# Kernel optimization log

Measured on AMD Instinct MI355X. Metric: run time of the kernel, lower is better.

Reference implementation:

```python
import jax, jax.numpy as jnp
import numpy as np
from jax import lax

B, N, T = 64, 50, 30          # batch, history length, words per title
VOCAB, E = 50000, 300          # vocab size, word emb dim
FN, A, G, K = 400, 200, 400, 3 # filter_num, attention_dim, gru_unit, window size
USERS = 50000


def setup_inputs() -> dict:
    key = jax.random.key(0)
    ks = jax.random.split(key, 12)
    return {
        "user_id": jax.random.randint(ks[0], (B,), 0, USERS),
        "history_title": jax.random.randint(ks[1], (B, N, T), 0, VOCAB),
        "history_length": jax.random.randint(ks[2], (B,), 1, N + 1),
        "word_emb": jax.random.normal(ks[3], (VOCAB, E), jnp.float32) * 0.02,
        "conv_w": jax.random.normal(ks[4], (K, E, FN), jnp.float32) * 0.05,  # WIO layout
        "conv_b": jnp.zeros((FN,), jnp.float32),
        "v": jax.random.normal(ks[5], (FN, A), jnp.float32) * 0.05,
        "vb": jnp.zeros((A,), jnp.float32),
        "q": jax.random.normal(ks[6], (A, 1), jnp.float32) * 0.05,
        "user_emb": jax.random.normal(ks[7], (USERS, G), jnp.float32) * 0.02,
        "W_ih": jax.random.normal(ks[8], (3 * G, FN), jnp.float32) * 0.05,
        "W_hh": jax.random.normal(ks[9], (3 * G, G), jnp.float32) * 0.05,
        "b_ih": jnp.zeros((3 * G,), jnp.float32),
        "b_hh": jnp.zeros((3 * G,), jnp.float32),
    }


def _news_encode(history_title, word_emb, conv_w, conv_b, v, vb, q):
    # word embedding lookup: [B, N, T, E] (dropout is identity in eval mode)
    W = word_emb[history_title]
    # Conv1d over the word axis, padding=1 keeps length T
    x = W.reshape(B * N, T, E)
    C = lax.conv_general_dilated(
        x, conv_w, window_strides=(1,), padding=[(1, 1)],
        dimension_numbers=("NWC", "WIO", "NWC")) + conv_b
    C = jax.nn.relu(C).reshape(B, N, T, FN)
    # additive attention scores
    a = jnp.tanh(jnp.einsum("bntf,fa->bnta", C, v) + vb)
    a = jnp.einsum("bnta,ao->bnt", a, q)  # q: [A,1] -> squeeze
    # original uses Softmax(dim=0) on a [n, t] per sample => over the n-titles axis
    alpha = jax.nn.softmax(a, axis=1)
    # e[i] = alpha[i] @ C[i]: weighted sum over words -> [B, N, FN]
    return jnp.einsum("bnt,bntf->bnf", alpha, C)


def _gru(news_embed, h0, lengths, W_ih, W_hh, b_ih, b_hh):
    # packed_padded semantics: h stops updating once step >= length
    xs = jnp.swapaxes(news_embed, 0, 1)                 # [N, B, FN]
    mask = jnp.arange(N)[:, None] < lengths[None, :]    # [N, B]

    def step(h, inp):
        x_t, m = inp
        gx = x_t @ W_ih.T + b_ih                        # [B, 3G]
        gh = h @ W_hh.T + b_hh
        xr, xz, xn = jnp.split(gx, 3, axis=-1)
        hr, hz, hn = jnp.split(gh, 3, axis=-1)
        r = jax.nn.sigmoid(xr + hr)
        z = jax.nn.sigmoid(xz + hz)
        n = jnp.tanh(xn + r * hn)
        h_new = (1.0 - z) * n + z * h
        h = jnp.where(m[:, None], h_new, h)
        return h, None

    h_final, _ = lax.scan(step, h0, (xs, mask))
    return h_final


def reference(user_id, history_title, history_length, word_emb, conv_w, conv_b,
              v, vb, q, user_emb, W_ih, W_hh, b_ih, b_hh):
    news_embed = _news_encode(history_title, word_emb, conv_w, conv_b, v, vb, q)
    h0 = user_emb[user_id]                              # [B, G]
    return _gru(news_embed, h0, history_length, W_ih, W_hh, b_ih, b_hh)
```

## Files before the change

### kernel.cpp

```cpp
#include <hip/hip_runtime.h>
#include <hip/hip_bf16.h>

#define BB 64
#define NN 50
#define TT 30
#define EE 300
#define FN 400
#define AA 200
#define GG 400

typedef __attribute__((ext_vector_type(8))) short bf16x8;
typedef __attribute__((ext_vector_type(4))) float f32x4;

__device__ inline ushort f2bf(float x) {
  __hip_bfloat16 b = __float2bfloat16(x);
  return *(ushort*)&b;
}

__global__ void k_prep_all(
    const float* __restrict__ Whh, const float* __restrict__ cw,
    const float* __restrict__ v, const float* __restrict__ q,
    const float* __restrict__ vb, const float* __restrict__ Wih,
    const int* __restrict__ user_id, const float* __restrict__ user_emb,
    float* __restrict__ Wpack, __hip_bfloat16* __restrict__ WT2,
    __hip_bfloat16* __restrict__ vT2, float* __restrict__ qp,
    float* __restrict__ vbp, __hip_bfloat16* __restrict__ Wih_bf,
    float* __restrict__ h0)
{
  int i = blockIdx.x * 256 + threadIdx.x;
  if (i < 480000) {
    int jl = i % 150;
    int g = (i / 150) % 400;
    int gc = i / 60000;
    int gate = jl / 50, gl = jl - gate * 50;
    int j = gate * 400 + gc * 50 + gl;
    Wpack[i] = Whh[j * 400 + g];
  } else if (i < 910080) {
    int k = i - 480000;
    int kk = k & 31, f = (k >> 5) % 448, s = k / (448 * 32);
    int ko = s / 10, e = (s - ko * 10) * 32 + kk;
    float val = (f < FN && e < EE) ? cw[(ko * EE + e) * FN + f] : 0.f;
    WT2[k] = __float2bfloat16(val);
  } else if (i < 1003264) {
    int k = i - 910080;
    int kk = k & 31, a = (k >> 5) % 224, ks = k / (224 * 32);
    int e = ks * 32 + kk;
    float val = (a < AA && e < FN) ? v[e * AA + a] : 0.f;
    vT2[k] = __float2bfloat16(val);
  } else if (i < 1003488) {
    int k = i - 1003264;
    qp[k]  = k < AA ? q[k]  : 0.f;
    vbp[k] = k < AA ? vb[k] : 0.f;
  } else if (i < 1562592) {
    int k = i - 1003488;
    int j = k / 416, f = k % 416;
    Wih_bf[k] = __float2bfloat16((j < 1200 && f < FN) ? Wih[j * 400 + f] : 0.f);
  } else if (i < 1588192) {
    int k = i - 1562592;
    int b = k / GG, g = k - b * GG;
    h0[k] = user_emb[(size_t)user_id[b] * GG + g];
  }
}

__global__ void k_prep_emb(const float* __restrict__ w, __hip_bfloat16* __restrict__ o) {
  int i = blockIdx.x * 256 + threadIdx.x;
  if (i < 50000 * 80) {
    int row = i / 80, cg = i - row * 80;
    ushort4 u4 = make_ushort4(0, 0, 0, 0);
    if (cg < 75) {
      float4 v4 = *(const float4*)(w + (size_t)row * EE + cg * 4);
      u4 = make_ushort4(f2bf(v4.x), f2bf(v4.y), f2bf(v4.z), f2bf(v4.w));
    }
    *(ushort4*)((ushort*)o + (size_t)row * 320 + cg * 4) = u4;
  }
}

__global__ __launch_bounds__(256, 2) void k_conv(
    const int* __restrict__ title, const __hip_bfloat16* __restrict__ emb,
    const __hip_bfloat16* __restrict__ WT2, const float* __restrict__ conv_b,
    __hip_bfloat16* __restrict__ C)
{
  __shared__ __align__(16) ushort E[2][34][332];
  __shared__ int words[60];
  const int g = blockIdx.x;
  const int tid = threadIdx.x;
  const int lane = tid & 63, wn = tid >> 6;
  const int l15 = lane & 15, l4 = lane >> 4;

  if (tid < 60) words[tid] = title[g * 60 + tid];
  for (int idx = tid; idx < 2822; idx += 256)
    *(uint4*)((ushort*)E + idx * 8) = make_uint4(0u, 0u, 0u, 0u);
  __syncthreads();
  for (int idx = tid; idx < 2400; idx += 256) {
    int row = idx / 40, c = idx - row * 40;
    int tt = row / 30, w = row - tt * 30;
    *(uint4*)(&E[tt][w + 1][c * 8]) =
        *(const uint4*)((const ushort*)emb + (size_t)words[row] * 320 + c * 8);
  }
  __syncthreads();

  f32x4 acc[4][7];
#pragma unroll
  for (int nt = 0; nt < 7; ++nt) {
    int f = wn * 112 + nt * 16 + l15;
    float bj = (f < FN) ? conv_b[f] : 0.f;
#pragma unroll
    for (int mt = 0; mt < 4; ++mt) {
      acc[mt][nt][0] = bj; acc[mt][nt][1] = bj;
      acc[mt][nt][2] = bj; acc[mt][nt][3] = bj;
    }
  }

  const ushort* Bbase = (const ushort*)WT2 + (size_t)(wn * 112 + l15) * 32 + l4 * 8;

#pragma unroll
  for (int ko = 0; ko < 3; ++ko) {
#pragma unroll
    for (int ks = 0; ks < 10; ++ks) {
      const int s = ko * 10 + ks;
      bf16x8 bq[7];
#pragma unroll
      for (int nt = 0; nt < 7; ++nt)
        bq[nt] = *(const bf16x8*)(Bbase + (size_t)s * 14336 + nt * 512);
      bf16x8 af[4];
#pragma unroll
      for (int mt = 0; mt < 4; ++mt)
        af[mt] = *(const bf16x8*)(&E[mt >> 1][(mt & 1) * 16 + l15 + ko][ks * 32 + l4 * 8]);
#pragma unroll
      for (int nt = 0; nt < 7; ++nt)
#pragma unroll
        for (int mt = 0; mt < 4; ++mt)
          acc[mt][nt] = __builtin_amdgcn_mfma_f32_16x16x32_bf16(af[mt], bq[nt], acc[mt][nt], 0, 0, 0);
    }
  }

#pragma unroll
  for (int mt = 0; mt < 4; ++mt) {
    const int ti = mt >> 1;
    const int tb = (mt & 1) * 16 + l4 * 4;
#pragma unroll
    for (int nt = 0; nt < 7; ++nt) {
      int f = wn * 112 + nt * 16 + l15;
      if (f < 416) {
#pragma unroll
        for (int r = 0; r < 4; ++r) {
          int t = tb + r;
          if (t < TT) {
            float vv = fmaxf(acc[mt][nt][r], 0.f);
            C[((size_t)(g * 2 + ti) * 30 + t) * 416 + f] = __float2bfloat16(vv);
          }
        }
      }
    }
  }
}

__global__ __launch_bounds__(512) void k_attn(
    const __hip_bfloat16* __restrict__ C, const __hip_bfloat16* __restrict__ vT2,
    const float* __restrict__ vbp, const float* __restrict__ qp,
    float* __restrict__ score)
{
  __shared__ float sred[2][256];
  const int tid = threadIdx.x;
  const int lane = tid & 63, wid = tid >> 6;
  const int wm = wid >> 1, wn = wid & 1;
  const int l15 = lane & 15, l4 = lane >> 4;
  const size_t row0 = (size_t)blockIdx.x * 256;

  f32x4 acc[4][7];
  float ql[7];
#pragma unroll
  for (int nt = 0; nt < 7; ++nt) {
    int a = wn * 112 + nt * 16 + l15;
    ql[nt] = qp[a];
    float vbv = vbp[a];
#pragma unroll
    for (int mt = 0; mt < 4; ++mt) {
      acc[mt][nt][0] = vbv; acc[mt][nt][1] = vbv;
      acc[mt][nt][2] = vbv; acc[mt][nt][3] = vbv;
    }
  }

  const ushort* Vbase = (const ushort*)vT2 + (size_t)(wn * 112 + l15) * 32 + l4 * 8;
  const ushort* Cbase = (const ushort*)C + (row0 + wm * 64 + l15) * 416 + l4 * 8;

  for (int ks = 0; ks < 13; ++ks) {
    bf16x8 vf[7];
#pragma unroll
    for (int nt = 0; nt < 7; ++nt)
      vf[nt] = *(const bf16x8*)(Vbase + ((size_t)ks * 224 + nt * 16) * 32);
    bf16x8 cf[4];
#pragma unroll
    for (int mt = 0; mt < 4; ++mt)
      cf[mt] = *(const bf16x8*)(Cbase + (size_t)mt * 16 * 416 + ks * 32);
#pragma unroll
    for (int nt = 0; nt < 7; ++nt)
#pragma unroll
      for (int mt = 0; mt < 4; ++mt)
        acc[mt][nt] = __builtin_amdgcn_mfma_f32_16x16x32_bf16(cf[mt], vf[nt], acc[mt][nt], 0, 0, 0);
  }

  float sums[4][4];
#pragma unroll
  for (int mt = 0; mt < 4; ++mt)
#pragma unroll
    for (int r = 0; r < 4; ++r) sums[mt][r] = 0.f;
#pragma unroll
  for (int mt = 0; mt < 4; ++mt)
#pragma unroll
    for (int nt = 0; nt < 7; ++nt)
#pragma unroll
      for (int r = 0; r < 4; ++r)
        sums[mt][r] += tanhf(acc[mt][nt][r]) * ql[nt];
#pragma unroll
  for (int mask = 1; mask < 16; mask <<= 1)
#pragma unroll
    for (int mt = 0; mt < 4; ++mt)
#pragma unroll
      for (int r = 0; r < 4; ++r)
        sums[mt][r] += __shfl_xor(sums[mt][r], mask);

  float outv = 0.f;
#pragma unroll
  for (int mt = 0; mt < 4; ++mt)
#pragma unroll
    for (int r = 0; r < 4; ++r)
      if (l15 == mt * 4 + r) outv = sums[mt][r];
  sred[wn][wm * 64 + (l15 >> 2) * 16 + l4 * 4 + (l15 & 3)] = outv;
  __syncthreads();
  if (tid < 256) score[row0 + tid] = sred[0][tid] + sred[1][tid];
}

__global__ void k2_softmax_n(const float* __restrict__ score, float* __restrict__ alpha) {
  int i = blockIdx.x * 256 + threadIdx.x;
  if (i >= BB * TT) return;
  int b = i / TT, t = i - b * TT;
  int base = b * (NN * TT) + t;
  float m = -1e30f;
  for (int n = 0; n < NN; ++n) m = fmaxf(m, score[base + n * TT]);
  float s = 0.f;
  for (int n = 0; n < NN; ++n) s += __expf(score[base + n * TT] - m);
  float inv = 1.f / s;
  for (int n = 0; n < NN; ++n)
    alpha[base + n * TT] = __expf(score[base + n * TT] - m) * inv;
}

__global__ __launch_bounds__(256) void k3_wsum(
    const float* __restrict__ alpha, const __hip_bfloat16* __restrict__ C,
    __hip_bfloat16* __restrict__ Ebf) {
  __shared__ float al[TT];
  const int bn = blockIdx.x;
  const int tid = threadIdx.x;
  if (tid < TT) al[tid] = alpha[bn * TT + tid];
  __syncthreads();
  for (int f = tid; f < 416; f += 256) {
    float s = 0.f;
    if (f < FN) {
#pragma unroll
      for (int t = 0; t < TT; ++t)
        s = fmaf(al[t], __bfloat162float(C[((size_t)bn * TT + t) * 416 + f]), s);
    }
    Ebf[(size_t)bn * 416 + f] = __float2bfloat16(s);
  }
}

__global__ __launch_bounds__(512) void k4_gx_mfma(
    const __hip_bfloat16* __restrict__ Ebf,
    const __hip_bfloat16* __restrict__ Wih,
    const float* __restrict__ b_ih,
    float* __restrict__ gx)
{
  __shared__ __align__(16) ushort Alds[128 * 40];
  __shared__ __align__(16) ushort Blds[448 * 40];
  const int tid = threadIdx.x;
  const int lane = tid & 63, wid = tid >> 6;
  const int wm = wid >> 2, wn = wid & 3;
  const int l15 = lane & 15, l4 = lane >> 4;
  const int mb = blockIdx.x / 3;
  const int nb = blockIdx.x - mb * 3;
  const int row0 = mb * 128;
  const int n0 = nb * 448;

  f32x4 acc[4][7];
#pragma unroll
  for (int nt = 0; nt < 7; ++nt) {
    int j = n0 + wn * 112 + nt * 16 + l15;
    float bj = (j < 1200) ? b_ih[j] : 0.f;
#pragma unroll
    for (int mt = 0; mt < 4; ++mt) {
      acc[mt][nt][0] = bj; acc[mt][nt][1] = bj;
      acc[mt][nt][2] = bj; acc[mt][nt][3] = bj;
    }
  }

  const int ar = tid >> 2, ac = tid & 3;
  for (int ks = 0; ks < 13; ++ks) {
    *(uint4*)(&Alds[ar * 40 + ac * 8]) =
        *(const uint4*)((const ushort*)Ebf + (size_t)(row0 + ar) * 416 + ks * 32 + ac * 8);
    for (int idx = tid; idx < 1792; idx += 512) {
      int r = idx >> 2, c = idx & 3;
      *(uint4*)(&Blds[r * 40 + c * 8]) =
          *(const uint4*)((const ushort*)Wih + (size_t)(n0 + r) * 416 + ks * 32 + c * 8);
    }
    __syncthreads();
    bf16x8 af[4];
#pragma unroll
    for (int mt = 0; mt < 4; ++mt)
      af[mt] = *(const bf16x8*)(&Alds[(wm * 64 + mt * 16 + l15) * 40 + l4 * 8]);
#pragma unroll
    for (int nt = 0; nt < 7; ++nt) {
      bf16x8 bfr = *(const bf16x8*)(&Blds[(wn * 112 + nt * 16 + l15) * 40 + l4 * 8]);
#pragma unroll
      for (int mt = 0; mt < 4; ++mt)
        acc[mt][nt] = __builtin_amdgcn_mfma_f32_16x16x32_bf16(af[mt], bfr, acc[mt][nt], 0, 0, 0);
    }
    __syncthreads();
  }

#pragma unroll
  for (int mt = 0; mt < 4; ++mt) {
    int row = row0 + wm * 64 + mt * 16 + l4 * 4;
#pragma unroll
    for (int nt = 0; nt < 7; ++nt) {
      int j = n0 + wn * 112 + nt * 16 + l15;
      if (j < 1200) {
#pragma unroll
        for (int r = 0; r < 4; ++r)
          gx[(size_t)(row + r) * 1200 + j] = acc[mt][nt][r];
      }
    }
  }
}

__global__ __launch_bounds__(256) void k5_step(
    const float* __restrict__ h_prev, float* __restrict__ h_next,
    const float* __restrict__ Wpack, const float* __restrict__ b_hh,
    const float* __restrict__ gx, const int* __restrict__ hist_len,
    float* __restrict__ out, int step)
{
  const int gc = blockIdx.x & 7;
  const int bg = blockIdx.x >> 3;
  const int tid = threadIdx.x;
  __shared__ float ghl[2][3][50];

  if (tid < 150) {
    const float* h0p = h_prev + (size_t)(2 * bg) * GG;
    const float* h1p = h0p + GG;
    float a00 = 0.f, a01 = 0.f, a10 = 0.f, a11 = 0.f;
    const float* wp = Wpack + (size_t)gc * 60000 + tid;
#pragma unroll 8
    for (int g = 0; g < 200; ++g) {
      float w0 = wp[g * 150];
      float w1 = wp[(g + 200) * 150];
      float h00 = h0p[g], h01 = h0p[g + 200];
      float h10 = h1p[g], h11 = h1p[g + 200];
      a00 = fmaf(h00, w0, a00);
      a10 = fmaf(h10, w0, a10);
      a01 = fmaf(h01, w1, a01);
      a11 = fmaf(h11, w1, a11);
    }
    int gate = tid / 50, gl = tid - gate * 50;
    float bb = b_hh[gate * 400 + gc * 50 + gl];
    ghl[0][gate][gl] = a00 + a01 + bb;
    ghl[1][gate][gl] = a10 + a11 + bb;
  }
  __syncthreads();

  if (tid < 100) {
    int b = tid / 50, gl = tid - (tid / 50) * 50;
    int babs = 2 * bg + b;
    int g = gc * 50 + gl;
    const float* gxp = gx + ((size_t)babs * NN + step) * 1200;
    float xr = gxp[g], xz = gxp[400 + g], xn = gxp[800 + g];
    float hr = ghl[b][0][gl], hz = ghl[b][1][gl], hn = ghl[b][2][gl];
    float r = 1.f / (1.f + __expf(-(xr + hr)));
    float z = 1.f / (1.f + __expf(-(xz + hz)));
    float nv = tanhf(xn + r * hn);
    float hold = h_prev[(size_t)babs * GG + g];
    float hnew = (1.f - z) * nv + z * hold;
    float hres = (step < hist_len[babs]) ? hnew : hold;
    h_next[(size_t)babs * GG + g] = hres;
    if (step == NN - 1) out[(size_t)babs * GG + g] = hres;
  }
}

extern "C" void kernel_launch(void* const* d_in, const int* in_sizes, int n_in,
                              void* d_out, int out_size, void* d_ws, size_t ws_size,
                              hipStream_t stream) {
  const int*   user_id   = (const int*)d_in[0];
  const int*   title     = (const int*)d_in[1];
  const int*   hist_len  = (const int*)d_in[2];
  const float* word_emb  = (const float*)d_in[3];
  const float* conv_w    = (const float*)d_in[4];
  const float* conv_b    = (const float*)d_in[5];
  const float* v         = (const float*)d_in[6];
  const float* vb        = (const float*)d_in[7];
  const float* q         = (const float*)d_in[8];
  const float* user_emb  = (const float*)d_in[9];
  const float* W_ih      = (const float*)d_in[10];
  const float* W_hh      = (const float*)d_in[11];
  const float* b_ih      = (const float*)d_in[12];
  const float* b_hh      = (const float*)d_in[13];
  float* out = (float*)d_out;

  char* ws = (char*)d_ws;
  size_t off = 0;
  auto take = [&](size_t bytes) {
    char* p = ws + off;
    off = (off + bytes + 255) & ~(size_t)255;
    return p;
  };
  __hip_bfloat16* C      = (__hip_bfloat16*)take((size_t)BB * NN * TT * 416 * 2);
  float* score  = (float*)take((size_t)BB * NN * TT * 4);
  float* alpha  = (float*)take((size_t)BB * NN * TT * 4);
  __hip_bfloat16* Ebf    = (__hip_bfloat16*)take((size_t)BB * NN * 416 * 2);
  __hip_bfloat16* Wih_bf = (__hip_bfloat16*)take((size_t)1344 * 416 * 2);
  float* Wpack  = (float*)take((size_t)8 * 400 * 150 * 4);
  float* gx     = (float*)take((size_t)BB * NN * 1200 * 4);
  float* h0     = (float*)take((size_t)BB * GG * 4);
  float* h1     = (float*)take((size_t)BB * GG * 4);
  __hip_bfloat16* emb_bf = (__hip_bfloat16*)take((size_t)50000 * 320 * 2);
  __hip_bfloat16* WT2    = (__hip_bfloat16*)take((size_t)30 * 448 * 32 * 2);
  __hip_bfloat16* vT2    = (__hip_bfloat16*)take((size_t)13 * 224 * 32 * 2);
  float* qp     = (float*)take(224 * 4);
  float* vbp    = (float*)take(224 * 4);
  (void)ws_size;

  k_prep_all<<<6204, 256, 0, stream>>>(W_hh, conv_w, v, q, vb, W_ih, user_id,
                                       user_emb, Wpack, WT2, vT2, qp, vbp,
                                       Wih_bf, h0);
  k_prep_emb<<<(50000 * 80 + 255) / 256, 256, 0, stream>>>(word_emb, emb_bf);

  k_conv<<<BB * NN / 2, 256, 0, stream>>>(title, emb_bf, WT2, conv_b, C);
  k_attn<<<BB * NN * TT / 256, 512, 0, stream>>>(C, vT2, vbp, qp, score);
  k2_softmax_n<<<(BB * TT + 255) / 256, 256, 0, stream>>>(score, alpha);
  k3_wsum<<<BB * NN, 256, 0, stream>>>(alpha, C, Ebf);
  k4_gx_mfma<<<75, 512, 0, stream>>>(Ebf, Wih_bf, b_ih, gx);

  float* hbuf[2] = {h0, h1};
  for (int step = 0; step < NN; ++step) {
    k5_step<<<256, 256, 0, stream>>>(hbuf[step & 1], hbuf[(step + 1) & 1],
                                     Wpack, b_hh, gx, hist_len, out, step);
  }
}
```

Measured before the change: 955.5 us.

## Fuse GRU time steps into one persistent kernel and stage attention tiles in LDS

The 50 per-step GRU launches become one kernel in which each block owns two batch rows and keeps the hidden state in shared memory across all steps. W_hh is stored transposed as [g][1200] so each thread reads float4 columns, and the h0 gather moves into this kernel. This removes launch overhead and the global round-trips of the hidden state, but only 32 blocks run and each streams the full W_hh every step, so the recurrence runs on far fewer CUs. Separately, k_attn now stages each C k-slice cooperatively in padded LDS before the MFMA loop, adding two barriers per k-step.

```diff
diff --git a/kernel.cpp b/kernel.cpp
--- a/kernel.cpp
+++ b/kernel.cpp
@@ -17,24 +17,20 @@
   return *(ushort*)&b;
 }
 
+__device__ inline float sigf(float x) { return 1.f / (1.f + __expf(-x)); }
+
 __global__ void k_prep_all(
     const float* __restrict__ Whh, const float* __restrict__ cw,
     const float* __restrict__ v, const float* __restrict__ q,
     const float* __restrict__ vb, const float* __restrict__ Wih,
-    const int* __restrict__ user_id, const float* __restrict__ user_emb,
-    float* __restrict__ Wpack, __hip_bfloat16* __restrict__ WT2,
+    float* __restrict__ WhhT, __hip_bfloat16* __restrict__ WT2,
     __hip_bfloat16* __restrict__ vT2, float* __restrict__ qp,
-    float* __restrict__ vbp, __hip_bfloat16* __restrict__ Wih_bf,
-    float* __restrict__ h0)
+    float* __restrict__ vbp, __hip_bfloat16* __restrict__ Wih_bf)
 {
   int i = blockIdx.x * 256 + threadIdx.x;
   if (i < 480000) {
-    int jl = i % 150;
-    int g = (i / 150) % 400;
-    int gc = i / 60000;
-    int gate = jl / 50, gl = jl - gate * 50;
-    int j = gate * 400 + gc * 50 + gl;
-    Wpack[i] = Whh[j * 400 + g];
+    int g = i / 1200, j = i - g * 1200;
+    WhhT[i] = Whh[j * 400 + g];
   } else if (i < 910080) {
     int k = i - 480000;
     int kk = k & 31, f = (k >> 5) % 448, s = k / (448 * 32);
@@ -55,10 +51,6 @@
     int k = i - 1003488;
     int j = k / 416, f = k % 416;
     Wih_bf[k] = __float2bfloat16((j < 1200 && f < FN) ? Wih[j * 400 + f] : 0.f);
-  } else if (i < 1588192) {
-    int k = i - 1562592;
-    int b = k / GG, g = k - b * GG;
-    h0[k] = user_emb[(size_t)user_id[b] * GG + g];
   }
 }
 
@@ -160,6 +152,7 @@
     const float* __restrict__ vbp, const float* __restrict__ qp,
     float* __restrict__ score)
 {
+  __shared__ __align__(16) ushort Clds[256 * 40];
   __shared__ float sred[2][256];
   const int tid = threadIdx.x;
   const int lane = tid & 63, wid = tid >> 6;
@@ -182,22 +175,28 @@
   }
 
   const ushort* Vbase = (const ushort*)vT2 + (size_t)(wn * 112 + l15) * 32 + l4 * 8;
-  const ushort* Cbase = (const ushort*)C + (row0 + wm * 64 + l15) * 416 + l4 * 8;
 
   for (int ks = 0; ks < 13; ++ks) {
     bf16x8 vf[7];
 #pragma unroll
     for (int nt = 0; nt < 7; ++nt)
       vf[nt] = *(const bf16x8*)(Vbase + ((size_t)ks * 224 + nt * 16) * 32);
+    for (int idx = tid; idx < 1024; idx += 512) {
+      int r = idx >> 2, c = idx & 3;
+      *(uint4*)(&Clds[r * 40 + c * 8]) =
+          *(const uint4*)((const ushort*)C + (row0 + r) * 416 + ks * 32 + c * 8);
+    }
+    __syncthreads();
     bf16x8 cf[4];
 #pragma unroll
     for (int mt = 0; mt < 4; ++mt)
-      cf[mt] = *(const bf16x8*)(Cbase + (size_t)mt * 16 * 416 + ks * 32);
+      cf[mt] = *(const bf16x8*)(&Clds[(wm * 64 + mt * 16 + l15) * 40 + l4 * 8]);
 #pragma unroll
     for (int nt = 0; nt < 7; ++nt)
 #pragma unroll
       for (int mt = 0; mt < 4; ++mt)
         acc[mt][nt] = __builtin_amdgcn_mfma_f32_16x16x32_bf16(cf[mt], vf[nt], acc[mt][nt], 0, 0, 0);
+    __syncthreads();
   }
 
   float sums[4][4];
@@ -332,55 +331,76 @@
   }
 }
 
-__global__ __launch_bounds__(256) void k5_step(
-    const float* __restrict__ h_prev, float* __restrict__ h_next,
-    const float* __restrict__ Wpack, const float* __restrict__ b_hh,
-    const float* __restrict__ gx, const int* __restrict__ hist_len,
-    float* __restrict__ out, int step)
+__global__ __launch_bounds__(320) void k5_gru(
+    const int* __restrict__ user_id, const int* __restrict__ hist_len,
+    const float* __restrict__ user_emb,
+    const float* __restrict__ WhhT,
+    const float* __restrict__ b_hh,
+    const float* __restrict__ gx,
+    float* __restrict__ out)
 {
-  const int gc = blockIdx.x & 7;
-  const int bg = blockIdx.x >> 3;
+  __shared__ float hl[2][GG];
+  __shared__ float gh[2][1200];
+  const int blk = blockIdx.x;
+  const int b0 = blk * 2;
   const int tid = threadIdx.x;
-  __shared__ float ghl[2][3][50];
-
-  if (tid < 150) {
-    const float* h0p = h_prev + (size_t)(2 * bg) * GG;
-    const float* h1p = h0p + GG;
-    float a00 = 0.f, a01 = 0.f, a10 = 0.f, a11 = 0.f;
-    const float* wp = Wpack + (size_t)gc * 60000 + tid;
-#pragma unroll 8
-    for (int g = 0; g < 200; ++g) {
-      float w0 = wp[g * 150];
-      float w1 = wp[(g + 200) * 150];
-      float h00 = h0p[g], h01 = h0p[g + 200];
-      float h10 = h1p[g], h11 = h1p[g + 200];
-      a00 = fmaf(h00, w0, a00);
-      a10 = fmaf(h10, w0, a10);
-      a01 = fmaf(h01, w1, a01);
-      a11 = fmaf(h11, w1, a11);
-    }
-    int gate = tid / 50, gl = tid - gate * 50;
-    float bb = b_hh[gate * 400 + gc * 50 + gl];
-    ghl[0][gate][gl] = a00 + a01 + bb;
-    ghl[1][gate][gl] = a10 + a11 + bb;
-  }
+
+  for (int i = tid; i < 2 * GG; i += 320) {
+    int b = i / GG, g = i - b * GG;
+    hl[b][g] = user_emb[(size_t)user_id[b0 + b] * GG + g];
+  }
+  const int len0 = hist_len[b0];
+  const int len1 = hist_len[b0 + 1];
+
+  const int j4 = tid * 4;
+  float4 bh4 = make_float4(0.f, 0.f, 0.f, 0.f);
+  if (tid < 300) bh4 = *(const float4*)(b_hh + j4);
   __syncthreads();
 
-  if (tid < 100) {
-    int b = tid / 50, gl = tid - (tid / 50) * 50;
-    int babs = 2 * bg + b;
-    int g = gc * 50 + gl;
-    const float* gxp = gx + ((size_t)babs * NN + step) * 1200;
-    float xr = gxp[g], xz = gxp[400 + g], xn = gxp[800 + g];
-    float hr = ghl[b][0][gl], hz = ghl[b][1][gl], hn = ghl[b][2][gl];
-    float r = 1.f / (1.f + __expf(-(xr + hr)));
-    float z = 1.f / (1.f + __expf(-(xz + hz)));
-    float nv = tanhf(xn + r * hn);
-    float hold = h_prev[(size_t)babs * GG + g];
-    float hnew = (1.f - z) * nv + z * hold;
-    float hres = (step < hist_len[babs]) ? hnew : hold;
-    h_next[(size_t)babs * GG + g] = hres;
-    if (step == NN - 1) out[(size_t)babs * GG + g] = hres;
+  for (int step = 0; step < NN; ++step) {
+    if (tid < 300) {
+      float a0x = 0.f, a0y = 0.f, a0z = 0.f, a0w = 0.f;
+      float a1x = 0.f, a1y = 0.f, a1z = 0.f, a1w = 0.f;
+      const float* wp = WhhT + j4;
+#pragma unroll 2
+      for (int g4 = 0; g4 < 100; ++g4) {
+        float4 h0v = *(const float4*)(&hl[0][g4 * 4]);
+        float4 h1v = *(const float4*)(&hl[1][g4 * 4]);
+#pragma unroll
+        for (int c = 0; c < 4; ++c) {
+          float4 w = *(const float4*)(wp + (size_t)(g4 * 4 + c) * 1200);
+          float h0 = (c == 0) ? h0v.x : (c == 1) ? h0v.y : (c == 2) ? h0v.z : h0v.w;
+          float h1 = (c == 0) ? h1v.x : (c == 1) ? h1v.y : (c == 2) ? h1v.z : h1v.w;
+          a0x = fmaf(w.x, h0, a0x); a0y = fmaf(w.y, h0, a0y);
+          a0z = fmaf(w.z, h0, a0z); a0w = fmaf(w.w, h0, a0w);
+          a1x = fmaf(w.x, h1, a1x); a1y = fmaf(w.y, h1, a1y);
+          a1z = fmaf(w.z, h1, a1z); a1w = fmaf(w.w, h1, a1w);
+        }
+      }
+      *(float4*)(&gh[0][j4]) = make_float4(a0x + bh4.x, a0y + bh4.y, a0z + bh4.z, a0w + bh4.w);
+      *(float4*)(&gh[1][j4]) = make_float4(a1x + bh4.x, a1y + bh4.y, a1z + bh4.z, a1w + bh4.w);
+    }
+    __syncthreads();
+
+    for (int i = tid; i < 800; i += 320) {
+      int b = i / 400, g = i - b * 400;
+      const float* gxp = gx + ((size_t)(b0 + b) * NN + step) * 1200;
+      float xr = gxp[g], xz = gxp[400 + g], xn = gxp[800 + g];
+      float hr = gh[b][g], hz = gh[b][400 + g], hn = gh[b][800 + g];
+      float r = sigf(xr + hr);
+      float z = sigf(xz + hz);
+      float nv = tanhf(xn + r * hn);
+      float hold = hl[b][g];
+      float hnew = (1.f - z) * nv + z * hold;
+      int len = b ? len1 : len0;
+      if (step < len) hl[b][g] = hnew;
+    }
+    __syncthreads();
+  }
+
+  for (int i = tid; i < 2 * GG; i += 320) {
+    int b = i / GG, g = i - b * GG;
+    out[(size_t)(b0 + b) * GG + g] = hl[b][g];
   }
 }
 
@@ -415,10 +435,8 @@
   float* alpha  = (float*)take((size_t)BB * NN * TT * 4);
   __hip_bfloat16* Ebf    = (__hip_bfloat16*)take((size_t)BB * NN * 416 * 2);
   __hip_bfloat16* Wih_bf = (__hip_bfloat16*)take((size_t)1344 * 416 * 2);
-  float* Wpack  = (float*)take((size_t)8 * 400 * 150 * 4);
+  float* WhhT   = (float*)take((size_t)400 * 1200 * 4);
   float* gx     = (float*)take((size_t)BB * NN * 1200 * 4);
-  float* h0     = (float*)take((size_t)BB * GG * 4);
-  float* h1     = (float*)take((size_t)BB * GG * 4);
   __hip_bfloat16* emb_bf = (__hip_bfloat16*)take((size_t)50000 * 320 * 2);
   __hip_bfloat16* WT2    = (__hip_bfloat16*)take((size_t)30 * 448 * 32 * 2);
   __hip_bfloat16* vT2    = (__hip_bfloat16*)take((size_t)13 * 224 * 32 * 2);
@@ -426,9 +444,8 @@
   float* vbp    = (float*)take(224 * 4);
   (void)ws_size;
 
-  k_prep_all<<<6204, 256, 0, stream>>>(W_hh, conv_w, v, q, vb, W_ih, user_id,
-                                       user_emb, Wpack, WT2, vT2, qp, vbp,
-                                       Wih_bf, h0);
+  k_prep_all<<<6104, 256, 0, stream>>>(W_hh, conv_w, v, q, vb, W_ih,
+                                       WhhT, WT2, vT2, qp, vbp, Wih_bf);
   k_prep_emb<<<(50000 * 80 + 255) / 256, 256, 0, stream>>>(word_emb, emb_bf);
 
   k_conv<<<BB * NN / 2, 256, 0, stream>>>(title, emb_bf, WT2, conv_b, C);
@@ -437,9 +454,6 @@
   k3_wsum<<<BB * NN, 256, 0, stream>>>(alpha, C, Ebf);
   k4_gx_mfma<<<75, 512, 0, stream>>>(Ebf, Wih_bf, b_ih, gx);
 
-  float* hbuf[2] = {h0, h1};
-  for (int step = 0; step < NN; ++step) {
-    k5_step<<<256, 256, 0, stream>>>(hbuf[step & 1], hbuf[(step + 1) & 1],
-                                     Wpack, b_hh, gx, hist_len, out, step);
-  }
-}
+  k5_gru<<<BB / 2, 320, 0, stream>>>(user_id, hist_len, user_emb, WhhT, b_hh,
+                                     gx, out);
+}
```

Result: slower. 1.123 ms (+17.5%).
